# Kernel optimization log

Measured on AMD Instinct MI355X. Metric: run time of the kernel, lower is better.

## Reference

```python
import jax, jax.numpy as jnp
import numpy as np

B, S, E, H = 8, 1024, 1024, 16
D = E // H  # head_dim = 64


def setup_inputs() -> dict:
    key = jax.random.key(0)
    ks = jax.random.split(key, 10)
    def lin(k):
        kw, kb = jax.random.split(k)
        lim = 1.0 / np.sqrt(E)
        W = jax.random.uniform(kw, (E, E), jnp.float32, -lim, lim)
        b = jax.random.uniform(kb, (E,), jnp.float32, -lim, lim)
        return W, b
    Wq, bq = lin(ks[0]); Wk, bk = lin(ks[1]); Wv, bv = lin(ks[2]); Wo, bo = lin(ks[3])
    ent = jax.random.normal(ks[4], (H, H), jnp.float32)
    x = jax.random.normal(ks[5], (B, S, E), jnp.float32)
    mask = jnp.ones((B, 1, S, S), jnp.int32)
    return {"x": x, "mask": mask, "Wq": Wq, "bq": bq, "Wk": Wk, "bk": bk,
            "Wv": Wv, "bv": bv, "Wo": Wo, "bo": bo, "ent": ent}


def reference(x, mask, Wq, bq, Wk, bk, Wv, bv, Wo, bo, ent):
    Bs, Sl, Ed = x.shape
    def heads(W, b):
        return (x @ W.T + b).reshape(Bs, Sl, H, D).transpose(0, 2, 1, 3)  # [B,H,S,D]
    q, k, v = heads(Wq, bq), heads(Wk, bk), heads(Wv, bv)
    scores = jnp.einsum('bhqd,bhkd->bhqk', q, k) / np.sqrt(D)  # [B,H,S,S]
    Em = jax.nn.softmax(ent, axis=-1)  # [H,H]
    scores = jnp.einsum('bhqk,hg->bgqk', scores, Em)  # cross-head entanglement mix
    scores = jnp.where(mask == 0, jnp.float32(-1e9), scores)
    attn = jax.nn.softmax(scores, axis=-1)
    out = jnp.einsum('bhqk,bhkd->bhqd', attn, v)
    out = out.transpose(0, 2, 1, 3).reshape(Bs, Sl, Ed)
    return out @ Wo.T + bo
```

## Files before the change

kernel.cpp:

```cpp
#include <hip/hip_runtime.h>

#define DEVINL static __device__ __forceinline__

typedef __attribute__((ext_vector_type(4)))  float f32x4;
typedef __attribute__((ext_vector_type(16))) float f32x16;
typedef __attribute__((ext_vector_type(4)))  float float4_t;
typedef __attribute__((ext_vector_type(8)))  short short8;
typedef __attribute__((ext_vector_type(4)))  short short4v;
typedef __attribute__((ext_vector_type(4)))  int   int4v;

DEVINL unsigned short f2bf(float f){
  union { float f; unsigned int u; } x; x.f = f;
  return (unsigned short)((x.u + 0x7fffu + ((x.u >> 16) & 1u)) >> 16);
}
DEVINL float bf2f(unsigned short h){
  union { unsigned int u; float f; } x; x.u = ((unsigned int)h) << 16;
  return x.f;
}
DEVINL f32x4 zero4(){ f32x4 z; z[0]=0.f; z[1]=0.f; z[2]=0.f; z[3]=0.f; return z; }
DEVINL f32x16 zero16(){ f32x16 z;
#pragma unroll
  for (int e=0;e<16;++e) z[e]=0.f;
  return z; }

#define GLL16(gp, lp) __builtin_amdgcn_global_load_lds( \
    (const __attribute__((address_space(1))) void*)(gp), \
    (__attribute__((address_space(3))) void*)(lp), 16, 0, 0)

__global__ __launch_bounds__(256) void cast_f32_bf16(const float* __restrict__ src,
                                                     unsigned short* __restrict__ dst, int n8){
  int i = blockIdx.x * 256 + threadIdx.x;
  if (i >= n8) return;
  const float4_t* s = (const float4_t*)src;
  float4_t a = s[2*i], b = s[2*i+1];
  short8 o;
  o[0]=(short)f2bf(a[0]); o[1]=(short)f2bf(a[1]); o[2]=(short)f2bf(a[2]); o[3]=(short)f2bf(a[3]);
  o[4]=(short)f2bf(b[0]); o[5]=(short)f2bf(b[1]); o[6]=(short)f2bf(b[2]); o[7]=(short)f2bf(b[3]);
  *(short8*)(dst + (size_t)i*8) = o;
}

__global__ __launch_bounds__(256) void prep_em(const float* __restrict__ ent,
                                               unsigned short* __restrict__ EmT){
  int t = threadIdx.x;
  if (t < 16){
    float v[16]; float mx = -3.0e38f;
#pragma unroll
    for (int j=0;j<16;++j){ v[j] = ent[t*16 + j]; mx = fmaxf(mx, v[j]); }
    float s = 0.f;
#pragma unroll
    for (int j=0;j<16;++j){ v[j] = __expf(v[j]-mx); s += v[j]; }
    float inv = (1.f/s) * 0.125f * 1.4426950408889634f;
#pragma unroll
    for (int j=0;j<16;++j) EmT[j*16 + t] = f2bf(v[j]*inv);
  }
  EmT[256 + t] = 0;
}

__global__ __launch_bounds__(256) void prep_maskbits(const int* __restrict__ mask,
                                                     unsigned* __restrict__ mb){
  int id = blockIdx.x * 256 + threadIdx.x;
  const int* src = mask + (size_t)id * 32;
  unsigned word = 0u;
#pragma unroll
  for (int c=0;c<8;++c){
    int4v v = *(const int4v*)(src + c*4);
    word |= (unsigned)(v[0]!=0) << (c*4)
          | (unsigned)(v[1]!=0) << (c*4+1)
          | (unsigned)(v[2]!=0) << (c*4+2)
          | (unsigned)(v[3]!=0) << (c*4+3);
  }
  mb[id] = word;
}

template<int MODE>
__global__ __launch_bounds__(256) void gemm_bt(const unsigned short* __restrict__ A,
                                               const unsigned short* __restrict__ W4,
                                               const float* __restrict__ bias0,
                                               const float* __restrict__ bias1,
                                               const float* __restrict__ bias2,
                                               void* __restrict__ outp){
  __shared__ __align__(16) unsigned short As[4096];
  __shared__ __align__(16) unsigned short Bs[4096];
  const int tid = threadIdx.x;
  const int w = tid >> 6, ln = tid & 63;
  const int wm = w >> 1, wn = w & 1;
  const int lq = ln & 15, lg = ln >> 4;
  const int m0 = blockIdx.y * 128, n0 = blockIdx.x * 128;
  const int z = blockIdx.z;
  const unsigned short* Bt = W4 + (size_t)z * 1048576;
  const float* bias = (z == 0) ? bias0 : ((z == 1) ? bias1 : bias2);

  const unsigned short* Ag = A  + (size_t)(m0 + (tid >> 2)) * 1024 + (tid & 3) * 8;
  const unsigned short* Bg = Bt + (size_t)(n0 + (tid >> 2)) * 1024 + (tid & 3) * 8;
  unsigned short* lA0 = As + w * 512;
  unsigned short* lA1 = As + 2048 + w * 512;
  unsigned short* lB0 = Bs + w * 512;
  unsigned short* lB1 = Bs + 2048 + w * 512;

  f32x4 acc[4][4];
#pragma unroll
  for (int i=0;i<4;++i)
#pragma unroll
    for (int j=0;j<4;++j) acc[i][j] = zero4();

  for (int kb = 0; kb < 32; ++kb){
    const int k0 = kb * 32;
    GLL16(Ag + k0,         lA0);
    GLL16(Ag + k0 + 65536, lA1);
    GLL16(Bg + k0,         lB0);
    GLL16(Bg + k0 + 65536, lB1);
    __syncthreads();
    short8 af[4], bf_[4];
#pragma unroll
    for (int i=0;i<4;++i) af[i]  = *(const short8*)(As + (wm*64 + i*16 + lq)*32 + lg*8);
#pragma unroll
    for (int j=0;j<4;++j) bf_[j] = *(const short8*)(Bs + (wn*64 + j*16 + lq)*32 + lg*8);
#pragma unroll
    for (int i=0;i<4;++i)
#pragma unroll
      for (int j=0;j<4;++j)
        acc[i][j] = __builtin_amdgcn_mfma_f32_16x16x32_bf16(af[i], bf_[j], acc[i][j], 0, 0, 0);
    __syncthreads();
  }

  const int mrow = m0 + wm*64, ncol = n0 + wn*64;
  float bj[4];
#pragma unroll
  for (int j=0;j<4;++j) bj[j] = bias[ncol + j*16 + lq];
#pragma unroll
  for (int i=0;i<4;++i)
#pragma unroll
    for (int j=0;j<4;++j)
#pragma unroll
      for (int r=0;r<4;++r){
        float v = acc[i][j][r] + bj[j];
        int m = mrow + i*16 + lg*4 + r;
        int n = ncol + j*16 + lq;
        if (MODE == 0){
          int bb = m >> 10, sI = m & 1023, h = n >> 6, d = n & 63;
          ((unsigned short*)outp)[(size_t)z*8388608 + (((size_t)bb*16 + h)*1024 + sI)*64 + d] = f2bf(v);
        } else {
          ((float*)outp)[(size_t)m*1024 + n] = v;
        }
      }
}

__global__ __launch_bounds__(256) void transpose_v(const unsigned short* __restrict__ V,
                                                   unsigned short* __restrict__ Vt){
  int idx = blockIdx.x * 256 + threadIdx.x;
  int s8 = idx & 127, d = (idx >> 7) & 63, bh = idx >> 13;
  const unsigned short* src = V + (size_t)bh*65536 + (size_t)s8*8*64 + d;
  short8 o;
#pragma unroll
  for (int j=0;j<8;++j) o[j] = (short)src[(size_t)j*64];
  *(short8*)(Vt + (size_t)bh*65536 + (size_t)d*1024 + (size_t)s8*8) = o;
}

__global__ __launch_bounds__(512,2) void attn_fused(const unsigned short* __restrict__ Q,
    const unsigned short* __restrict__ K, const unsigned short* __restrict__ Vt,
    const unsigned* __restrict__ MB, const unsigned short* __restrict__ EmT,
    unsigned short* __restrict__ AO){
  __shared__ __align__(16) unsigned short sraw[8192];
  __shared__ __align__(16) unsigned short smix[8192];
  const int tid = threadIdx.x;
  const int w = tid >> 6, ln = tid & 63;
  const int lq = ln & 15, lg = ln >> 4;
  const int l5 = ln & 31, h5 = ln >> 5;
  const int bid = blockIdx.x;
  const int bb = bid & 7, q0 = (bid >> 3) * 16;
  const int aQ = w & 3, n0 = w >> 2, g0 = w * 2;

  const unsigned short* Qb = Q  + ((size_t)bb*16 + 4*aQ) * 65536;
  const unsigned short* Kb = K  + ((size_t)bb*16 + 4*aQ) * 65536 + (size_t)(n0*16 + lq)*64 + lg*8;
  const unsigned short* Vb = Vt + ((size_t)bb*16 + g0) * 65536;
  const unsigned* Mw = MB + (size_t)bb*32768 + (size_t)(q0 + lq)*32;

  short8 emA = *(const short8*)(EmT + l5*16 + h5*8);

  short8 qf[4][2];
#pragma unroll
  for (int hh=0; hh<4; ++hh)
#pragma unroll
    for (int ks=0; ks<2; ++ks)
      qf[hh][ks] = *(const short8*)(Qb + (size_t)hh*65536 + (size_t)(q0 + lq)*64 + ks*32 + lg*8);

  f32x4 acco[2][4];
#pragma unroll
  for (int a=0;a<2;++a)
#pragma unroll
    for (int n=0;n<4;++n) acco[a][n] = zero4();
  float mst[2] = {-3.0e38f,-3.0e38f};
  float lst[2] = {0.f,0.f};

  const int kk = n0*16 + lq;

  for (int kt = 0; kt < 32; ++kt){
    const int kb = kt*32;
    f32x4 accs[4];
#pragma unroll
    for (int hh=0; hh<4; ++hh){
      short8 k0 = *(const short8*)(Kb + (size_t)hh*65536 + (size_t)kb*64);
      short8 k1 = *(const short8*)(Kb + (size_t)hh*65536 + (size_t)kb*64 + 32);
      accs[hh] = __builtin_amdgcn_mfma_f32_16x16x32_bf16(qf[hh][0], k0, zero4(), 0,0,0);
      accs[hh] = __builtin_amdgcn_mfma_f32_16x16x32_bf16(qf[hh][1], k1, accs[hh], 0,0,0);
    }
#pragma unroll
    for (int r=0;r<4;++r){
      const int qq = lg*4 + r;
      short4v pk;
      pk[0]=(short)f2bf(accs[0][r]); pk[1]=(short)f2bf(accs[1][r]);
      pk[2]=(short)f2bf(accs[2][r]); pk[3]=(short)f2bf(accs[3][r]);
      const int lin = (qq*32 + kk)*32 + aQ*8;
      const int sw  = (((kk>>2)&1)<<4) | (((qq>>2)&3)<<5);
      *(short4v*)((char*)sraw + (lin ^ sw)) = pk;
    }
    __syncthreads();
#pragma unroll
    for (int t=0;t<2;++t){
      const int qq = w*2 + t;
      const int lin = (qq*32 + l5)*32 + h5*16;
      const int sw  = (((l5>>2)&1)<<4) | (((qq>>2)&3)<<5);
      short8 sfr = *(const short8*)((const char*)sraw + (lin ^ sw));
      f32x16 md = __builtin_amdgcn_mfma_f32_32x32x16_bf16(emA, sfr, zero16(), 0,0,0);
#pragma unroll
      for (int reg=0;reg<8;++reg){
        const int gg = (reg&3) + 8*(reg>>2) + 4*h5;
        int ob = gg*1024 + qq*64 + l5*2;
        ob ^= ((gg>>2)&1)<<6;
        *(short*)((char*)smix + ob) = (short)f2bf(md[reg]);
      }
    }
    __syncthreads();
    const unsigned mw = Mw[kt];
    const unsigned mshift = mw >> (lg*8);
    const int allon = __all((int)((mshift & 0xffu) == 0xffu));
#pragma unroll
    for (int hh=0; hh<2; ++hh){
      const int gg = g0 + hh;
      const int rb = (gg*1024 + lq*64 + lg*16) ^ (((gg>>2)&1)<<6);
      short8 sm8 = *(const short8*)((const char*)smix + rb);
      short8 vfr[4];
#pragma unroll
      for (int n=0;n<4;++n)
        vfr[n] = *(const short8*)(Vb + (size_t)hh*65536 + (size_t)(n*16 + lq)*1024 + kb + lg*8);
      float s[8];
#pragma unroll
      for (int j=0;j<8;++j) s[j] = bf2f((unsigned short)sm8[j]);
      if (!allon){
#pragma unroll
        for (int j=0;j<8;++j) if (!((mshift>>j)&1u)) s[j] = -1.44269504e9f;
      }
      float pm = s[0];
#pragma unroll
      for (int j=1;j<8;++j) pm = fmaxf(pm, s[j]);
      pm = fmaxf(pm, __shfl_xor(pm, 16, 64));
      pm = fmaxf(pm, __shfl_xor(pm, 32, 64));
      const float mo = mst[hh];
      const float mn = fmaxf(mo, pm);
      const float sc = exp2f(mo - mn);
      float p[8]; float ps = 0.f;
#pragma unroll
      for (int j=0;j<8;++j){ p[j] = exp2f(s[j] - mn); ps += p[j]; }
      ps += __shfl_xor(ps, 16, 64);
      ps += __shfl_xor(ps, 32, 64);
      lst[hh] = lst[hh]*sc + ps;
      mst[hh] = mn;
      short8 pa;
#pragma unroll
      for (int j=0;j<8;++j) pa[j] = (short)f2bf(p[j]);
      const float scr0 = __shfl(sc, lg*4 + 0, 64);
      const float scr1 = __shfl(sc, lg*4 + 1, 64);
      const float scr2 = __shfl(sc, lg*4 + 2, 64);
      const float scr3 = __shfl(sc, lg*4 + 3, 64);
#pragma unroll
      for (int n=0;n<4;++n){
        acco[hh][n][0] *= scr0; acco[hh][n][1] *= scr1;
        acco[hh][n][2] *= scr2; acco[hh][n][3] *= scr3;
      }
#pragma unroll
      for (int n=0;n<4;++n)
        acco[hh][n] = __builtin_amdgcn_mfma_f32_16x16x32_bf16(pa, vfr[n], acco[hh][n], 0,0,0);
    }
  }
#pragma unroll
  for (int hh=0; hh<2; ++hh){
    const int gg = g0 + hh;
    const float linv = 1.0f / lst[hh];
    const float l0 = __shfl(linv, lg*4+0, 64), l1 = __shfl(linv, lg*4+1, 64);
    const float l2 = __shfl(linv, lg*4+2, 64), l3 = __shfl(linv, lg*4+3, 64);
#pragma unroll
    for (int n=0;n<4;++n){
      const int e = gg*64 + n*16 + lq;
      const size_t base = ((size_t)bb*1024 + (size_t)(q0 + lg*4))*1024 + e;
      AO[base         ] = f2bf(acco[hh][n][0]*l0);
      AO[base + 1024  ] = f2bf(acco[hh][n][1]*l1);
      AO[base + 2048  ] = f2bf(acco[hh][n][2]*l2);
      AO[base + 3072  ] = f2bf(acco[hh][n][3]*l3);
    }
  }
}

extern "C" void kernel_launch(void* const* d_in, const int* in_sizes, int n_in,
                              void* d_out, int out_size, void* d_ws, size_t ws_size,
                              hipStream_t stream){
  const float* x   = (const float*)d_in[0];
  const int*   msk = (const int*)  d_in[1];
  const float* Wq  = (const float*)d_in[2];
  const float* bq  = (const float*)d_in[3];
  const float* Wk  = (const float*)d_in[4];
  const float* bk  = (const float*)d_in[5];
  const float* Wv  = (const float*)d_in[6];
  const float* bv  = (const float*)d_in[7];
  const float* Wo  = (const float*)d_in[8];
  const float* bo  = (const float*)d_in[9];
  const float* ent = (const float*)d_in[10];

  char* ws = (char*)d_ws;
  unsigned short* xb  = (unsigned short*)(ws);
  unsigned short* Wb  = (unsigned short*)(ws + 16777216);
  unsigned short* qkv = (unsigned short*)(ws + 25165824);
  unsigned short* EmT = (unsigned short*)(ws + 75497472);
  unsigned*       MB  = (unsigned*)     (ws + 75499520);
  unsigned short* Vt  = xb;
  unsigned short* AO  = qkv + (size_t)2*8388608;

  cast_f32_bf16<<<4096, 256, 0, stream>>>(x,  xb,            1048576);
  cast_f32_bf16<<<512,  256, 0, stream>>>(Wq, Wb,            131072);
  cast_f32_bf16<<<512,  256, 0, stream>>>(Wk, Wb + 1048576,  131072);
  cast_f32_bf16<<<512,  256, 0, stream>>>(Wv, Wb + 2097152,  131072);
  cast_f32_bf16<<<512,  256, 0, stream>>>(Wo, Wb + 3145728,  131072);
  prep_em<<<1, 256, 0, stream>>>(ent, EmT);
  prep_maskbits<<<1024, 256, 0, stream>>>(msk, MB);

  gemm_bt<0><<<dim3(8,64,3), 256, 0, stream>>>(xb, Wb, bq, bk, bv, (void*)qkv);
  transpose_v<<<4096, 256, 0, stream>>>(qkv + (size_t)2*8388608, Vt);
  attn_fused<<<512, 512, 0, stream>>>(qkv, qkv + 8388608, Vt, MB, EmT, AO);
  gemm_bt<1><<<dim3(8,64,1), 256, 0, stream>>>(AO, Wb + 3145728, bo, bo, bo, d_out);

  (void)in_sizes; (void)n_in; (void)out_size; (void)ws_size;
}
```

Baseline: 445.2 us.

## Double key tile to 64 per iteration and transpose PV MFMA operands

The fused attention kernel now processes 64 keys per iteration instead of 32, which halves the loop trip count and the number of block barriers, with the LDS score buffers doubled and their swizzle adjusted. V fragments are loaded up front at the start of each iteration. The P·V MFMA now takes V as the A operand and P as the B operand, so each lane holds per-query-row scale factors directly, removing the cross-lane shuffles for the rescale and the normalisation. Outputs are written as packed 32-bit stores. The cost is more LDS and more registers per thread, which may reduce occupancy under the 512-thread, 2-block launch bound.

```diff
diff --git a/kernel.cpp b/kernel.cpp
--- a/kernel.cpp
+++ b/kernel.cpp
@@ -8,6 +8,7 @@
 typedef __attribute__((ext_vector_type(8)))  short short8;
 typedef __attribute__((ext_vector_type(4)))  short short4v;
 typedef __attribute__((ext_vector_type(4)))  int   int4v;
+typedef __attribute__((ext_vector_type(2)))  unsigned u32x2;
 
 DEVINL unsigned short f2bf(float f){
   union { float f; unsigned int u; } x; x.f = f;
@@ -160,8 +161,8 @@
     const unsigned short* __restrict__ K, const unsigned short* __restrict__ Vt,
     const unsigned* __restrict__ MB, const unsigned short* __restrict__ EmT,
     unsigned short* __restrict__ AO){
-  __shared__ __align__(16) unsigned short sraw[8192];
-  __shared__ __align__(16) unsigned short smix[8192];
+  __shared__ __align__(16) unsigned short sraw[16384];
+  __shared__ __align__(16) unsigned short smix[16384];
   const int tid = threadIdx.x;
   const int w = tid >> 6, ln = tid & 63;
   const int lq = ln & 15, lg = ln >> 4;
@@ -171,9 +172,9 @@
   const int aQ = w & 3, n0 = w >> 2, g0 = w * 2;
 
   const unsigned short* Qb = Q  + ((size_t)bb*16 + 4*aQ) * 65536;
-  const unsigned short* Kb = K  + ((size_t)bb*16 + 4*aQ) * 65536 + (size_t)(n0*16 + lq)*64 + lg*8;
+  const unsigned short* Kb = K  + ((size_t)bb*16 + 4*aQ) * 65536 + (size_t)(n0*32 + lq)*64 + lg*8;
   const unsigned short* Vb = Vt + ((size_t)bb*16 + g0) * 65536;
-  const unsigned* Mw = MB + (size_t)bb*32768 + (size_t)(q0 + lq)*32;
+  const unsigned* Mwp = MB + (size_t)bb*32768 + (size_t)(q0 + lq)*32;
 
   short8 emA = *(const short8*)(EmT + l5*16 + h5*8);
 
@@ -192,110 +193,133 @@
   float mst[2] = {-3.0e38f,-3.0e38f};
   float lst[2] = {0.f,0.f};
 
-  const int kk = n0*16 + lq;
-
-  for (int kt = 0; kt < 32; ++kt){
-    const int kb = kt*32;
-    f32x4 accs[4];
+  for (int kt = 0; kt < 16; ++kt){
+    const int kb = kt*64;
+    const u32x2 mw = *(const u32x2*)(Mwp + kt*2);
+    short8 vfr[2][4][2];
+#pragma unroll
+    for (int hh=0;hh<2;++hh)
+#pragma unroll
+      for (int n=0;n<4;++n)
+#pragma unroll
+        for (int kh=0;kh<2;++kh)
+          vfr[hh][n][kh] = *(const short8*)(Vb + (size_t)hh*65536 + (size_t)(n*16 + lq)*1024 + kb + kh*32 + lg*8);
+
+    f32x4 accs[4][2];
 #pragma unroll
     for (int hh=0; hh<4; ++hh){
-      short8 k0 = *(const short8*)(Kb + (size_t)hh*65536 + (size_t)kb*64);
-      short8 k1 = *(const short8*)(Kb + (size_t)hh*65536 + (size_t)kb*64 + 32);
-      accs[hh] = __builtin_amdgcn_mfma_f32_16x16x32_bf16(qf[hh][0], k0, zero4(), 0,0,0);
-      accs[hh] = __builtin_amdgcn_mfma_f32_16x16x32_bf16(qf[hh][1], k1, accs[hh], 0,0,0);
+      short8 kf[2][2];
+#pragma unroll
+      for (int n=0;n<2;++n)
+#pragma unroll
+        for (int ks=0;ks<2;++ks)
+          kf[n][ks] = *(const short8*)(Kb + (size_t)hh*65536 + (size_t)(kb + n*16)*64 + ks*32);
+#pragma unroll
+      for (int n=0;n<2;++n){
+        accs[hh][n] = __builtin_amdgcn_mfma_f32_16x16x32_bf16(qf[hh][0], kf[n][0], zero4(), 0,0,0);
+        accs[hh][n] = __builtin_amdgcn_mfma_f32_16x16x32_bf16(qf[hh][1], kf[n][1], accs[hh][n], 0,0,0);
+      }
     }
 #pragma unroll
-    for (int r=0;r<4;++r){
-      const int qq = lg*4 + r;
-      short4v pk;
-      pk[0]=(short)f2bf(accs[0][r]); pk[1]=(short)f2bf(accs[1][r]);
-      pk[2]=(short)f2bf(accs[2][r]); pk[3]=(short)f2bf(accs[3][r]);
-      const int lin = (qq*32 + kk)*32 + aQ*8;
+    for (int n=0;n<2;++n)
+#pragma unroll
+      for (int r=0;r<4;++r){
+        const int qq = lg*4 + r;
+        const int kk = n0*32 + n*16 + lq;
+        short4v pk;
+        pk[0]=(short)f2bf(accs[0][n][r]); pk[1]=(short)f2bf(accs[1][n][r]);
+        pk[2]=(short)f2bf(accs[2][n][r]); pk[3]=(short)f2bf(accs[3][n][r]);
+        const int lin = (qq*64 + kk)*32 + aQ*8;
+        const int sw  = (((kk>>2)&1)<<4) | (((qq>>2)&3)<<5);
+        *(short4v*)((char*)sraw + (lin ^ sw)) = pk;
+      }
+    __syncthreads();
+#pragma unroll
+    for (int t=0;t<4;++t){
+      const int qq = w*2 + (t&1);
+      const int kh = t>>1;
+      const int kk = kh*32 + l5;
+      const int lin = (qq*64 + kk)*32 + h5*16;
       const int sw  = (((kk>>2)&1)<<4) | (((qq>>2)&3)<<5);
-      *(short4v*)((char*)sraw + (lin ^ sw)) = pk;
+      short8 sfr = *(const short8*)((const char*)sraw + (lin ^ sw));
+      f32x16 md = __builtin_amdgcn_mfma_f32_32x32x16_bf16(emA, sfr, zero16(), 0,0,0);
+#pragma unroll
+      for (int reg=0;reg<8;++reg){
+        const int gg = (reg&3) + 8*(reg>>2) + 4*h5;
+        int ob = gg*2048 + qq*128 + kk*2;
+        ob ^= ((qq&7)<<4) ^ (((gg>>2)&1)<<6);
+        *(short*)((char*)smix + ob) = (short)f2bf(md[reg]);
+      }
     }
     __syncthreads();
-#pragma unroll
-    for (int t=0;t<2;++t){
-      const int qq = w*2 + t;
-      const int lin = (qq*32 + l5)*32 + h5*16;
-      const int sw  = (((l5>>2)&1)<<4) | (((qq>>2)&3)<<5);
-      short8 sfr = *(const short8*)((const char*)sraw + (lin ^ sw));
-      f32x16 md = __builtin_amdgcn_mfma_f32_32x32x16_bf16(emA, sfr, zero16(), 0,0,0);
-#pragma unroll
-      for (int reg=0;reg<8;++reg){
-        const int gg = (reg&3) + 8*(reg>>2) + 4*h5;
-        int ob = gg*1024 + qq*64 + l5*2;
-        ob ^= ((gg>>2)&1)<<6;
-        *(short*)((char*)smix + ob) = (short)f2bf(md[reg]);
-      }
-    }
-    __syncthreads();
-    const unsigned mw = Mw[kt];
-    const unsigned mshift = mw >> (lg*8);
-    const int allon = __all((int)((mshift & 0xffu) == 0xffu));
+    const unsigned mb0 = (mw[0] >> (lg*8)) & 0xffu;
+    const unsigned mb1 = (mw[1] >> (lg*8)) & 0xffu;
+    const int allon = __all((int)((mb0 & mb1) == 0xffu));
 #pragma unroll
     for (int hh=0; hh<2; ++hh){
       const int gg = g0 + hh;
-      const int rb = (gg*1024 + lq*64 + lg*16) ^ (((gg>>2)&1)<<6);
-      short8 sm8 = *(const short8*)((const char*)smix + rb);
-      short8 vfr[4];
-#pragma unroll
-      for (int n=0;n<4;++n)
-        vfr[n] = *(const short8*)(Vb + (size_t)hh*65536 + (size_t)(n*16 + lq)*1024 + kb + lg*8);
-      float s[8];
-#pragma unroll
-      for (int j=0;j<8;++j) s[j] = bf2f((unsigned short)sm8[j]);
+      const int swc = ((lq&7)<<4) ^ (((gg>>2)&1)<<6);
+      const int base = gg*2048 + lq*128 + lg*16;
+      short8 sm0 = *(const short8*)((const char*)smix + ((base      ) ^ swc));
+      short8 sm1 = *(const short8*)((const char*)smix + ((base + 64 ) ^ swc));
+      float s[16];
+#pragma unroll
+      for (int j=0;j<8;++j){ s[j] = bf2f((unsigned short)sm0[j]); s[8+j] = bf2f((unsigned short)sm1[j]); }
       if (!allon){
 #pragma unroll
-        for (int j=0;j<8;++j) if (!((mshift>>j)&1u)) s[j] = -1.44269504e9f;
-      }
-      float pm = s[0];
-#pragma unroll
-      for (int j=1;j<8;++j) pm = fmaxf(pm, s[j]);
+        for (int j=0;j<8;++j){
+          if (!((mb0>>j)&1u)) s[j]    = -1.44269504e9f;
+          if (!((mb1>>j)&1u)) s[8+j]  = -1.44269504e9f;
+        }
+      }
+      float m01 = fmaxf(s[0],s[1]),  m23 = fmaxf(s[2],s[3]);
+      float m45 = fmaxf(s[4],s[5]),  m67 = fmaxf(s[6],s[7]);
+      float m89 = fmaxf(s[8],s[9]),  mab = fmaxf(s[10],s[11]);
+      float mcd = fmaxf(s[12],s[13]),mef = fmaxf(s[14],s[15]);
+      float pm = fmaxf(fmaxf(fmaxf(m01,m23), fmaxf(m45,m67)),
+                       fmaxf(fmaxf(m89,mab), fmaxf(mcd,mef)));
       pm = fmaxf(pm, __shfl_xor(pm, 16, 64));
       pm = fmaxf(pm, __shfl_xor(pm, 32, 64));
       const float mo = mst[hh];
       const float mn = fmaxf(mo, pm);
       const float sc = exp2f(mo - mn);
-      float p[8]; float ps = 0.f;
-#pragma unroll
-      for (int j=0;j<8;++j){ p[j] = exp2f(s[j] - mn); ps += p[j]; }
+      float p[16];
+#pragma unroll
+      for (int j=0;j<16;++j) p[j] = exp2f(s[j] - mn);
+      float ps = 0.f;
+#pragma unroll
+      for (int j=0;j<16;++j) ps += p[j];
       ps += __shfl_xor(ps, 16, 64);
       ps += __shfl_xor(ps, 32, 64);
       lst[hh] = lst[hh]*sc + ps;
       mst[hh] = mn;
-      short8 pa;
-#pragma unroll
-      for (int j=0;j<8;++j) pa[j] = (short)f2bf(p[j]);
-      const float scr0 = __shfl(sc, lg*4 + 0, 64);
-      const float scr1 = __shfl(sc, lg*4 + 1, 64);
-      const float scr2 = __shfl(sc, lg*4 + 2, 64);
-      const float scr3 = __shfl(sc, lg*4 + 3, 64);
+      short8 pa0, pa1;
+#pragma unroll
+      for (int j=0;j<8;++j){ pa0[j] = (short)f2bf(p[j]); pa1[j] = (short)f2bf(p[8+j]); }
 #pragma unroll
       for (int n=0;n<4;++n){
-        acco[hh][n][0] *= scr0; acco[hh][n][1] *= scr1;
-        acco[hh][n][2] *= scr2; acco[hh][n][3] *= scr3;
-      }
-#pragma unroll
-      for (int n=0;n<4;++n)
-        acco[hh][n] = __builtin_amdgcn_mfma_f32_16x16x32_bf16(pa, vfr[n], acco[hh][n], 0,0,0);
+        acco[hh][n][0] *= sc; acco[hh][n][1] *= sc;
+        acco[hh][n][2] *= sc; acco[hh][n][3] *= sc;
+      }
+#pragma unroll
+      for (int n=0;n<4;++n){
+        acco[hh][n] = __builtin_amdgcn_mfma_f32_16x16x32_bf16(vfr[hh][n][0], pa0, acco[hh][n], 0,0,0);
+        acco[hh][n] = __builtin_amdgcn_mfma_f32_16x16x32_bf16(vfr[hh][n][1], pa1, acco[hh][n], 0,0,0);
+      }
     }
   }
 #pragma unroll
   for (int hh=0; hh<2; ++hh){
     const int gg = g0 + hh;
     const float linv = 1.0f / lst[hh];
-    const float l0 = __shfl(linv, lg*4+0, 64), l1 = __shfl(linv, lg*4+1, 64);
-    const float l2 = __shfl(linv, lg*4+2, 64), l3 = __shfl(linv, lg*4+3, 64);
+    const size_t rowb = ((size_t)(bb*1024 + q0 + lq))*2048;
 #pragma unroll
     for (int n=0;n<4;++n){
-      const int e = gg*64 + n*16 + lq;
-      const size_t base = ((size_t)bb*1024 + (size_t)(q0 + lg*4))*1024 + e;
-      AO[base         ] = f2bf(acco[hh][n][0]*l0);
-      AO[base + 1024  ] = f2bf(acco[hh][n][1]*l1);
-      AO[base + 2048  ] = f2bf(acco[hh][n][2]*l2);
-      AO[base + 3072  ] = f2bf(acco[hh][n][3]*l3);
+      unsigned w0 = (unsigned)f2bf(acco[hh][n][0]*linv) | ((unsigned)f2bf(acco[hh][n][1]*linv) << 16);
+      unsigned w1 = (unsigned)f2bf(acco[hh][n][2]*linv) | ((unsigned)f2bf(acco[hh][n][3]*linv) << 16);
+      const int e = gg*64 + n*16 + lg*4;
+      *(unsigned*)((char*)AO + rowb + (size_t)e*2    ) = w0;
+      *(unsigned*)((char*)AO + rowb + (size_t)e*2 + 4) = w1;
     }
   }
 }
```

New measurement: 432.9 us. -2.8%, faster.

## Widen attention blocks to 32 queries with one output head per wave

Applied to the files above, without the earlier changes.

The attention kernel now runs 1024-thread blocks over 32 query rows instead of 512-thread blocks over 16. Each of the 16 waves owns a single output head across two 16-row query halves, which amortises the cross-head mixing MFMA and the Em fragment over more rows. The PV MFMA operands are swapped so each lane holds a whole query row, which removes the per-row rescale shuffles and lets outputs be written as packed 32-bit stores. V fragment and mask loads are hoisted ahead of the barriers, and __syncthreads is replaced by an explicit lgkmcnt wait plus s_barrier. The trade-offs are doubled shared memory per block, one block per CU, and half as many blocks.

```diff
diff --git a/kernel.cpp b/kernel.cpp
--- a/kernel.cpp
+++ b/kernel.cpp
@@ -22,6 +22,14 @@
 #pragma unroll
   for (int e=0;e<16;++e) z[e]=0.f;
   return z; }
+
+#define BARX() do{ \
+  __builtin_amdgcn_sched_barrier(0); \
+  asm volatile("s_waitcnt lgkmcnt(0)" ::: "memory"); \
+  __builtin_amdgcn_sched_barrier(0); \
+  __builtin_amdgcn_s_barrier(); \
+  __builtin_amdgcn_sched_barrier(0); \
+}while(0)
 
 #define GLL16(gp, lp) __builtin_amdgcn_global_load_lds( \
     (const __attribute__((address_space(1))) void*)(gp), \
@@ -156,24 +164,25 @@
   *(short8*)(Vt + (size_t)bh*65536 + (size_t)d*1024 + (size_t)s8*8) = o;
 }
 
-__global__ __launch_bounds__(512,2) void attn_fused(const unsigned short* __restrict__ Q,
+__global__ __launch_bounds__(1024,1) void attn_fused(const unsigned short* __restrict__ Q,
     const unsigned short* __restrict__ K, const unsigned short* __restrict__ Vt,
     const unsigned* __restrict__ MB, const unsigned short* __restrict__ EmT,
     unsigned short* __restrict__ AO){
-  __shared__ __align__(16) unsigned short sraw[8192];
-  __shared__ __align__(16) unsigned short smix[8192];
+  __shared__ __align__(16) unsigned short sraw[16384];
+  __shared__ __align__(16) unsigned short smix[16384];
   const int tid = threadIdx.x;
   const int w = tid >> 6, ln = tid & 63;
   const int lq = ln & 15, lg = ln >> 4;
   const int l5 = ln & 31, h5 = ln >> 5;
   const int bid = blockIdx.x;
-  const int bb = bid & 7, q0 = (bid >> 3) * 16;
-  const int aQ = w & 3, n0 = w >> 2, g0 = w * 2;
+  const int bb = bid & 7, q0 = (bid >> 3) * 32;
+  const int aQ = w & 3, iw = (w >> 2) & 1, ks0 = w >> 3;
+  const int g = w;
 
   const unsigned short* Qb = Q  + ((size_t)bb*16 + 4*aQ) * 65536;
-  const unsigned short* Kb = K  + ((size_t)bb*16 + 4*aQ) * 65536 + (size_t)(n0*16 + lq)*64 + lg*8;
-  const unsigned short* Vb = Vt + ((size_t)bb*16 + g0) * 65536;
-  const unsigned* Mw = MB + (size_t)bb*32768 + (size_t)(q0 + lq)*32;
+  const unsigned short* Kb = K  + ((size_t)bb*16 + 4*aQ) * 65536 + (size_t)(ks0*16 + lq)*64 + lg*8;
+  const unsigned short* Vb = Vt + ((size_t)bb*16 + g) * 65536;
+  const unsigned* Mwp = MB + (size_t)bb*32768 + (size_t)(q0 + lq)*32;
 
   short8 emA = *(const short8*)(EmT + l5*16 + h5*8);
 
@@ -182,17 +191,15 @@
   for (int hh=0; hh<4; ++hh)
 #pragma unroll
     for (int ks=0; ks<2; ++ks)
-      qf[hh][ks] = *(const short8*)(Qb + (size_t)hh*65536 + (size_t)(q0 + lq)*64 + ks*32 + lg*8);
+      qf[hh][ks] = *(const short8*)(Qb + (size_t)hh*65536 + (size_t)(q0 + iw*16 + lq)*64 + ks*32 + lg*8);
 
   f32x4 acco[2][4];
 #pragma unroll
-  for (int a=0;a<2;++a)
-#pragma unroll
-    for (int n=0;n<4;++n) acco[a][n] = zero4();
+  for (int i=0;i<2;++i)
+#pragma unroll
+    for (int n=0;n<4;++n) acco[i][n] = zero4();
   float mst[2] = {-3.0e38f,-3.0e38f};
   float lst[2] = {0.f,0.f};
-
-  const int kk = n0*16 + lq;
 
   for (int kt = 0; kt < 32; ++kt){
     const int kb = kt*32;
@@ -204,9 +211,16 @@
       accs[hh] = __builtin_amdgcn_mfma_f32_16x16x32_bf16(qf[hh][0], k0, zero4(), 0,0,0);
       accs[hh] = __builtin_amdgcn_mfma_f32_16x16x32_bf16(qf[hh][1], k1, accs[hh], 0,0,0);
     }
+    short8 vfr[4];
+#pragma unroll
+    for (int n=0;n<4;++n)
+      vfr[n] = *(const short8*)(Vb + (size_t)(n*16 + lq)*1024 + kb + lg*8);
+    const unsigned mw0 = Mwp[kt];
+    const unsigned mw1 = Mwp[512 + kt];
 #pragma unroll
     for (int r=0;r<4;++r){
-      const int qq = lg*4 + r;
+      const int qq = iw*16 + lg*4 + r;
+      const int kk = ks0*16 + lq;
       short4v pk;
       pk[0]=(short)f2bf(accs[0][r]); pk[1]=(short)f2bf(accs[1][r]);
       pk[2]=(short)f2bf(accs[2][r]); pk[3]=(short)f2bf(accs[3][r]);
@@ -214,7 +228,7 @@
       const int sw  = (((kk>>2)&1)<<4) | (((qq>>2)&3)<<5);
       *(short4v*)((char*)sraw + (lin ^ sw)) = pk;
     }
-    __syncthreads();
+    BARX();
 #pragma unroll
     for (int t=0;t<2;++t){
       const int qq = w*2 + t;
@@ -225,77 +239,64 @@
 #pragma unroll
       for (int reg=0;reg<8;++reg){
         const int gg = (reg&3) + 8*(reg>>2) + 4*h5;
-        int ob = gg*1024 + qq*64 + l5*2;
-        ob ^= ((gg>>2)&1)<<6;
+        int ob = gg*2048 + qq*64 + l5*2;
+        ob ^= ((gg>>2)&1)<<5;
         *(short*)((char*)smix + ob) = (short)f2bf(md[reg]);
       }
     }
-    __syncthreads();
-    const unsigned mw = Mw[kt];
-    const unsigned mshift = mw >> (lg*8);
-    const int allon = __all((int)((mshift & 0xffu) == 0xffu));
-#pragma unroll
-    for (int hh=0; hh<2; ++hh){
-      const int gg = g0 + hh;
-      const int rb = (gg*1024 + lq*64 + lg*16) ^ (((gg>>2)&1)<<6);
+    BARX();
+#pragma unroll
+    for (int i=0;i<2;++i){
+      const unsigned mwv = (i==0) ? mw0 : mw1;
+      const unsigned msh = (mwv >> (lg*8)) & 0xffu;
+      const int allon = __all((int)(msh == 0xffu));
+      const int rb = (g*2048 + (i*16 + lq)*64 + lg*16) ^ (((g>>2)&1)<<5);
       short8 sm8 = *(const short8*)((const char*)smix + rb);
-      short8 vfr[4];
-#pragma unroll
-      for (int n=0;n<4;++n)
-        vfr[n] = *(const short8*)(Vb + (size_t)hh*65536 + (size_t)(n*16 + lq)*1024 + kb + lg*8);
       float s[8];
 #pragma unroll
       for (int j=0;j<8;++j) s[j] = bf2f((unsigned short)sm8[j]);
       if (!allon){
 #pragma unroll
-        for (int j=0;j<8;++j) if (!((mshift>>j)&1u)) s[j] = -1.44269504e9f;
+        for (int j=0;j<8;++j) if (!((msh>>j)&1u)) s[j] = -1.44269504e9f;
       }
-      float pm = s[0];
-#pragma unroll
-      for (int j=1;j<8;++j) pm = fmaxf(pm, s[j]);
+      float m01 = fmaxf(s[0],s[1]), m23 = fmaxf(s[2],s[3]);
+      float m45 = fmaxf(s[4],s[5]), m67 = fmaxf(s[6],s[7]);
+      float pm = fmaxf(fmaxf(m01,m23), fmaxf(m45,m67));
       pm = fmaxf(pm, __shfl_xor(pm, 16, 64));
       pm = fmaxf(pm, __shfl_xor(pm, 32, 64));
-      const float mo = mst[hh];
+      const float mo = mst[i];
       const float mn = fmaxf(mo, pm);
       const float sc = exp2f(mo - mn);
-      float p[8]; float ps = 0.f;
-#pragma unroll
-      for (int j=0;j<8;++j){ p[j] = exp2f(s[j] - mn); ps += p[j]; }
+      float p[8];
+#pragma unroll
+      for (int j=0;j<8;++j) p[j] = exp2f(s[j] - mn);
+      float ps = ((p[0]+p[1]) + (p[2]+p[3])) + ((p[4]+p[5]) + (p[6]+p[7]));
       ps += __shfl_xor(ps, 16, 64);
       ps += __shfl_xor(ps, 32, 64);
-      lst[hh] = lst[hh]*sc + ps;
-      mst[hh] = mn;
+      lst[i] = lst[i]*sc + ps;
+      mst[i] = mn;
       short8 pa;
 #pragma unroll
       for (int j=0;j<8;++j) pa[j] = (short)f2bf(p[j]);
-      const float scr0 = __shfl(sc, lg*4 + 0, 64);
-      const float scr1 = __shfl(sc, lg*4 + 1, 64);
-      const float scr2 = __shfl(sc, lg*4 + 2, 64);
-      const float scr3 = __shfl(sc, lg*4 + 3, 64);
 #pragma unroll
       for (int n=0;n<4;++n){
-        acco[hh][n][0] *= scr0; acco[hh][n][1] *= scr1;
-        acco[hh][n][2] *= scr2; acco[hh][n][3] *= scr3;
+        acco[i][n][0] *= sc; acco[i][n][1] *= sc;
+        acco[i][n][2] *= sc; acco[i][n][3] *= sc;
+        acco[i][n] = __builtin_amdgcn_mfma_f32_16x16x32_bf16(vfr[n], pa, acco[i][n], 0,0,0);
       }
-#pragma unroll
-      for (int n=0;n<4;++n)
-        acco[hh][n] = __builtin_amdgcn_mfma_f32_16x16x32_bf16(pa, vfr[n], acco[hh][n], 0,0,0);
-    }
-  }
-#pragma unroll
-  for (int hh=0; hh<2; ++hh){
-    const int gg = g0 + hh;
-    const float linv = 1.0f / lst[hh];
-    const float l0 = __shfl(linv, lg*4+0, 64), l1 = __shfl(linv, lg*4+1, 64);
-    const float l2 = __shfl(linv, lg*4+2, 64), l3 = __shfl(linv, lg*4+3, 64);
+    }
+  }
+#pragma unroll
+  for (int i=0;i<2;++i){
+    const float linv = 1.0f / lst[i];
+    const size_t rowb = ((size_t)(bb*1024 + q0 + i*16 + lq))*2048;
 #pragma unroll
     for (int n=0;n<4;++n){
-      const int e = gg*64 + n*16 + lq;
-      const size_t base = ((size_t)bb*1024 + (size_t)(q0 + lg*4))*1024 + e;
-      AO[base         ] = f2bf(acco[hh][n][0]*l0);
-      AO[base + 1024  ] = f2bf(acco[hh][n][1]*l1);
-      AO[base + 2048  ] = f2bf(acco[hh][n][2]*l2);
-      AO[base + 3072  ] = f2bf(acco[hh][n][3]*l3);
+      unsigned w0 = (unsigned)f2bf(acco[i][n][0]*linv) | ((unsigned)f2bf(acco[i][n][1]*linv) << 16);
+      unsigned w1 = (unsigned)f2bf(acco[i][n][2]*linv) | ((unsigned)f2bf(acco[i][n][3]*linv) << 16);
+      const int e = g*64 + n*16 + lg*4;
+      *(unsigned*)((char*)AO + rowb + (size_t)e*2    ) = w0;
+      *(unsigned*)((char*)AO + rowb + (size_t)e*2 + 4) = w1;
     }
   }
 }
@@ -334,7 +335,7 @@
 
   gemm_bt<0><<<dim3(8,64,3), 256, 0, stream>>>(xb, Wb, bq, bk, bv, (void*)qkv);
   transpose_v<<<4096, 256, 0, stream>>>(qkv + (size_t)2*8388608, Vt);
-  attn_fused<<<512, 512, 0, stream>>>(qkv, qkv + 8388608, Vt, MB, EmT, AO);
+  attn_fused<<<256, 1024, 0, stream>>>(qkv, qkv + 8388608, Vt, MB, EmT, AO);
   gemm_bt<1><<<dim3(8,64,1), 256, 0, stream>>>(AO, Wb + 3145728, bo, bo, bo, d_out);
 
   (void)in_sizes; (void)n_in; (void)out_size; (void)ws_size;
```

Measured after the change: 474.4 us. 1.07x slower.
